# Performance work log

Hardware: AMD Instinct MI355X
Metric: run time of the kernel (lower is better)

Reference implementation:

```python
import jax, jax.numpy as jnp
import numpy as np

EPS_LN = 1e-5
EPS_STD = 1e-5


def _ln_dim1(z, g, b):
    # LayerNorm over channel dim (axis=1) of (B, C, T) or (B, C, 1)
    mu = z.mean(axis=1, keepdims=True)
    var = ((z - mu) ** 2).mean(axis=1, keepdims=True)
    return (z - mu) * jax.lax.rsqrt(var + EPS_LN) * g[None, :, None] + b[None, :, None]


def _stats(x, m):
    # weighted mean/std over time axis; m broadcasts over channels
    mean = (m * x).sum(axis=2)                                   # (B, C)
    std = jnp.sqrt(jnp.maximum((m * x * x).sum(axis=2) - mean ** 2, EPS_STD))
    return mean, std


def setup_inputs() -> dict:
    key = jax.random.key(0)
    ks = jax.random.split(key, 4)
    B, C, T, H = 16, 1536, 2000, 128
    x = jax.random.normal(ks[0], (B, C, T), dtype=jnp.float32)
    mask = jnp.ones((B, 1, T), dtype=jnp.float32)
    # attention MLP params (conv1x1 -> relu -> LN(dim=1) -> tanh -> conv1x1)
    w1 = jax.random.normal(ks[1], (H, 3 * C), dtype=jnp.float32) * (1.0 / np.sqrt(3 * C))
    b1 = jnp.zeros((H,), jnp.float32)
    g1 = jnp.ones((H,), jnp.float32)
    be1 = jnp.zeros((H,), jnp.float32)
    w2 = jax.random.normal(ks[2], (C, H), dtype=jnp.float32) * (1.0 / np.sqrt(H))
    b2 = jnp.zeros((C,), jnp.float32)
    g2 = jnp.ones((2 * C,), jnp.float32)
    be2 = jnp.zeros((2 * C,), jnp.float32)
    return {"x": x, "mask": mask, "w1": w1, "b1": b1, "g1": g1, "be1": be1,
            "w2": w2, "b2": b2, "g2": g2, "be2": be2}


def reference(x, mask, w1, b1, g1, be1, w2, b2, g2, be2):
    B, C, T = x.shape
    # time_attention: append masked global mean/std, broadcast over T
    total = mask.sum(axis=2, keepdims=True)                      # (B,1,1)
    mean0, std0 = _stats(x, mask / total)                        # (B,C)
    x_in = jnp.concatenate([
        x,
        jnp.broadcast_to(mean0[:, :, None], (B, C, T)),
        jnp.broadcast_to(std0[:, :, None], (B, C, T)),
    ], axis=1)                                                   # (B,3C,T)
    # attention MLP (conv1x1 == channel matmul)
    h = jnp.einsum("hc,bct->bht", w1, x_in) + b1[None, :, None]  # (B,H,T)
    h = jnp.tanh(_ln_dim1(jax.nn.relu(h), g1, be1))
    alpha = jnp.einsum("ch,bht->bct", w2, h) + b2[None, :, None]  # (B,C,T)
    # masked softmax over time
    alpha = jnp.where(mask == 0, -jnp.inf, alpha)
    alpha = jax.nn.softmax(alpha, axis=2)
    # attention-weighted stats
    mean, std = _stats(x, alpha)                                 # (B,C) each
    out = jnp.concatenate([mean, std], axis=1)[:, :, None]       # (B,2C,1)
    return _ln_dim1(out, g2, be2)
```

## Files before the change

kernel.cpp:

```cpp
#include <hip/hip_runtime.h>
#include <hip/hip_bf16.h>
#include <math.h>

constexpr int B_  = 16;
constexpr int C_  = 1536;
constexpr int T_  = 2000;
constexpr int H_  = 128;
constexpr int C3_ = 3 * C_;
constexpr int C2_ = 2 * C_;
constexpr int NT_ = 4;
constexpr int NTL_ = 32;

typedef short bf8 __attribute__((ext_vector_type(8)));
typedef short bf4 __attribute__((ext_vector_type(4)));
typedef float f4  __attribute__((ext_vector_type(4)));

__device__ inline unsigned short f2b(float f) {
  __bf16 h = (__bf16)f;
  return __builtin_bit_cast(unsigned short, h);
}

__global__ __launch_bounds__(256) void k_gemm1_stats(
    const float* __restrict__ x, const float* __restrict__ w1,
    const float* __restrict__ mask,
    float* __restrict__ h_pre, float* __restrict__ sp1, float* __restrict__ sp2) {
  __shared__ __align__(16) short As[2][128 * 32];
  __shared__ __align__(16) short Bs[2][64 * 32];
  const int b = blockIdx.y;
  const int tile = blockIdx.x;
  const int t0 = tile * 64;
  const int tid = threadIdx.x;
  const int lane = tid & 63;
  const int w = tid >> 6;
  const int l15 = lane & 15;
  const int l4 = lane >> 4;

  float4 va[4], vb[2];

  const int t4 = tid & 15;
  float mreg[4];
#pragma unroll
  for (int j = 0; j < 4; ++j) {
    int t = t0 + t4 * 4 + j;
    mreg[j] = (t < T_) ? mask[(size_t)b * T_ + t] : 0.f;
  }
  float* sp1row = sp1 + ((size_t)b * NTL_ + tile) * C_;
  float* sp2row = sp2 + ((size_t)b * NTL_ + tile) * C_;

  f4 acc[8];
#pragma unroll
  for (int mi = 0; mi < 8; ++mi) { f4 z = {0.f, 0.f, 0.f, 0.f}; acc[mi] = z; }

#define G1_GLOAD(K0)                                                          \
  {                                                                           \
    _Pragma("unroll")                                                         \
    for (int q = 0; q < 4; ++q) {                                             \
      int idx = q * 256 + tid;                                                \
      int row = idx >> 3, j4 = idx & 7;                                       \
      va[q] = *(const float4*)(w1 + (size_t)row * C3_ + (K0) + j4 * 4);       \
    }                                                                         \
    _Pragma("unroll")                                                         \
    for (int q = 0; q < 2; ++q) {                                             \
      int idx = q * 256 + tid;                                                \
      int k = idx >> 4;                                                       \
      int t = t0 + t4 * 4;                                                    \
      if (t < T_)                                                             \
        vb[q] = *(const float4*)(x + ((size_t)(b * C_ + (K0) + k)) * T_ + t); \
      else                                                                    \
        vb[q] = make_float4(0.f, 0.f, 0.f, 0.f);                              \
    }                                                                         \
  }
#define G1_LSTORE(BUF)                                                        \
  {                                                                           \
    _Pragma("unroll")                                                         \
    for (int q = 0; q < 4; ++q) {                                             \
      int idx = q * 256 + tid;                                                \
      int row = idx >> 3, j4 = idx & 7;                                       \
      int slot = (j4 >> 1) ^ ((row >> 2) & 3);                                \
      bf4 p;                                                                  \
      p[0] = (short)f2b(va[q].x); p[1] = (short)f2b(va[q].y);                 \
      p[2] = (short)f2b(va[q].z); p[3] = (short)f2b(va[q].w);                 \
      *(bf4*)&As[BUF][row * 32 + slot * 8 + (j4 & 1) * 4] = p;                \
    }                                                                         \
    _Pragma("unroll")                                                         \
    for (int q = 0; q < 2; ++q) {                                             \
      int idx = q * 256 + tid;                                                \
      int k = idx >> 4;                                                       \
      float vv[4] = {vb[q].x, vb[q].y, vb[q].z, vb[q].w};                     \
      _Pragma("unroll")                                                       \
      for (int j = 0; j < 4; ++j) {                                           \
        int row = t4 * 4 + j;                                                 \
        int slot = (k >> 3) ^ ((row >> 2) & 3);                               \
        Bs[BUF][row * 32 + slot * 8 + (k & 7)] = (short)f2b(vv[j]);           \
      }                                                                       \
    }                                                                         \
  }
#define G1_STATS(K0)                                                          \
  {                                                                           \
    _Pragma("unroll")                                                         \
    for (int q = 0; q < 2; ++q) {                                             \
      float vv[4] = {vb[q].x, vb[q].y, vb[q].z, vb[q].w};                     \
      float a1 = 0.f, a2 = 0.f;                                               \
      _Pragma("unroll")                                                       \
      for (int j = 0; j < 4; ++j) {                                           \
        float mx = mreg[j] * vv[j];                                           \
        a1 += mx;                                                             \
        a2 = fmaf(mx, vv[j], a2);                                             \
      }                                                                       \
      _Pragma("unroll")                                                       \
      for (int off = 1; off < 16; off <<= 1) {                                \
        a1 += __shfl_xor(a1, off);                                            \
        a2 += __shfl_xor(a2, off);                                            \
      }                                                                       \
      if (t4 == 0) {                                                          \
        int c = (K0) + q * 16 + (tid >> 4);                                   \
        sp1row[c] = a1;                                                       \
        sp2row[c] = a2;                                                       \
      }                                                                       \
    }                                                                         \
  }

  G1_GLOAD(0);
  G1_LSTORE(0);
  G1_STATS(0);
  __syncthreads();

  const int fA = (l15 >> 2) & 3;
  const int NS = C_ / 32;
  for (int s = 0; s < NS; ++s) {
    const int cur = s & 1;
    if (s + 1 < NS) G1_GLOAD((s + 1) * 32);
    {
      const int browB = w * 16 + l15;
      bf8 bfr = *(const bf8*)&Bs[cur][browB * 32 + (l4 ^ fA) * 8];
#pragma unroll
      for (int mi = 0; mi < 8; ++mi) {
        bf8 afr = *(const bf8*)&As[cur][(mi * 16 + l15) * 32 + (l4 ^ fA) * 8];
        acc[mi] = __builtin_amdgcn_mfma_f32_16x16x32_bf16(afr, bfr, acc[mi], 0, 0, 0);
      }
    }
    if (s + 1 < NS) {
      G1_LSTORE(cur ^ 1);
      G1_STATS((s + 1) * 32);
    }
    __syncthreads();
  }

  const int t = t0 + w * 16 + l15;
  if (t < T_) {
    float* dst = h_pre + ((size_t)b * T_ + t) * H_;
#pragma unroll
    for (int mi = 0; mi < 8; ++mi)
      *(f4*)&dst[mi * 16 + l4 * 4] = acc[mi];
  }
}

__global__ __launch_bounds__(256) void k_stats_reduce(
    const float* __restrict__ sp1, const float* __restrict__ sp2,
    const float* __restrict__ mask,
    float* __restrict__ mean0, float* __restrict__ std0) {
  __shared__ float rs[4];
  const int b = blockIdx.x / (C_ / 256);
  const int chunk = blockIdx.x % (C_ / 256);
  const int tid = threadIdx.x;
  const int lane = tid & 63;
  const int wv = tid >> 6;
  float sm = 0.f;
  for (int i = tid; i < T_; i += 256) sm += mask[(size_t)b * T_ + i];
#pragma unroll
  for (int off = 32; off; off >>= 1) sm += __shfl_xor(sm, off);
  if (lane == 0) rs[wv] = sm;
  __syncthreads();
  sm = rs[0] + rs[1] + rs[2] + rs[3];

  const int c = chunk * 256 + tid;
  float s1 = 0.f, s2 = 0.f;
#pragma unroll 8
  for (int tile = 0; tile < NTL_; ++tile) {
    const size_t j = ((size_t)b * NTL_ + tile) * C_ + c;
    s1 += sp1[j];
    s2 += sp2[j];
  }
  float mean = s1 / sm;
  float var = s2 / sm - mean * mean;
  mean0[b * C_ + c] = mean;
  std0[b * C_ + c] = sqrtf(fmaxf(var, 1e-5f));
}

__global__ __launch_bounds__(256) void k_hconst_wl1(
    const float* __restrict__ w1, const float* __restrict__ b1,
    const float* __restrict__ mean0, const float* __restrict__ std0,
    const float* __restrict__ w2,
    float* __restrict__ hconst, float* __restrict__ wl1) {
  const int wave = threadIdx.x >> 6;
  const int lane = threadIdx.x & 63;
  if (blockIdx.x < B_ * H_ / 4) {
    const int idx = blockIdx.x * 4 + wave;
    const int b = idx >> 7;
    const int h = idx & (H_ - 1);
    const float* wm  = w1 + (size_t)h * C3_ + C_;
    const float* wsd = wm + C_;
    const float* mn = mean0 + b * C_;
    const float* sd = std0 + b * C_;
    float s = 0.f;
    for (int c = lane; c < C_; c += 64)
      s += wm[c] * mn[c] + wsd[c] * sd[c];
#pragma unroll
    for (int off = 32; off; off >>= 1) s += __shfl_xor(s, off);
    if (lane == 0) hconst[idx] = s + b1[h];
  } else {
    const int c = (blockIdx.x - B_ * H_ / 4) * 4 + wave;
    const float* wr = w2 + (size_t)c * H_;
    float s = fabsf(wr[lane]) + fabsf(wr[lane + 64]);
#pragma unroll
    for (int off = 32; off; off >>= 1) s += __shfl_xor(s, off);
    if (lane == 0) wl1[c] = s;
  }
}

__global__ __launch_bounds__(256) void k_ln_epi(
    const float* __restrict__ h_pre, const float* __restrict__ hconst,
    const float* __restrict__ g1, const float* __restrict__ be1,
    unsigned short* __restrict__ hlnT) {
  const int b = blockIdx.y;
  const int t = blockIdx.x * 64 + (threadIdx.x >> 2);
  const int part = threadIdx.x & 3;
  if (t >= T_) return;
  const float* src = h_pre + ((size_t)b * T_ + t) * H_ + part * 32;
  const float* hc = hconst + b * H_ + part * 32;
  float v[32];
  float sum = 0.f, ssq = 0.f;
#pragma unroll
  for (int j = 0; j < 8; ++j) {
    float4 h4 = *(const float4*)(src + j * 4);
    float4 c4 = *(const float4*)(hc + j * 4);
    const float* hp = (const float*)&h4;
    const float* cp = (const float*)&c4;
#pragma unroll
    for (int r = 0; r < 4; ++r) {
      float u = fmaxf(hp[r] + cp[r], 0.f);
      v[j * 4 + r] = u;
      sum += u;
      ssq += u * u;
    }
  }
  sum += __shfl_xor(sum, 1); sum += __shfl_xor(sum, 2);
  ssq += __shfl_xor(ssq, 1); ssq += __shfl_xor(ssq, 2);
  const float mean = sum * (1.f / 128.f);
  const float rstd = rsqrtf(ssq * (1.f / 128.f) - mean * mean + 1e-5f);
  unsigned short* dst = hlnT + ((size_t)b * T_ + t) * H_ + part * 32;
  const float* gp = g1 + part * 32;
  const float* ep = be1 + part * 32;
#pragma unroll
  for (int m = 0; m < 4; ++m) {
    bf8 p;
#pragma unroll
    for (int r = 0; r < 8; ++r) {
      int j = m * 8 + r;
      p[r] = (short)f2b(tanhf((v[j] - mean) * rstd * gp[j] + ep[j]));
    }
    *(bf8*)&dst[m * 8] = p;
  }
}

__global__ __launch_bounds__(256) void k_gemm2_pool(
    const float* __restrict__ x, const float* __restrict__ mask,
    const float* __restrict__ w2, const unsigned short* __restrict__ hlnT,
    const float* __restrict__ wl1,
    float* __restrict__ ps0, float* __restrict__ ps1, float* __restrict__ ps2) {
  __shared__ __align__(16) short Hs[2][64 * 128];
  const int b = blockIdx.y;
  const int c0 = blockIdx.x * 128;
  const int part = blockIdx.z;
  const int tb = part * 512;
  const int te = min(tb + 512, T_);
  const int tid = threadIdx.x;
  const int lane = tid & 63;
  const int w = tid >> 6;
  const int l15 = lane & 15;
  const int l4 = lane >> 4;

  bf8 af[2][4];
#pragma unroll
  for (int mi = 0; mi < 2; ++mi)
#pragma unroll
    for (int ks = 0; ks < 4; ++ks) {
      const float* src = w2 + (size_t)(c0 + w * 32 + mi * 16 + l15) * H_ + (ks * 4 + l4) * 8;
      float4 v0 = *(const float4*)src;
      float4 v1 = *(const float4*)(src + 4);
      bf8 p;
      p[0] = (short)f2b(v0.x); p[1] = (short)f2b(v0.y);
      p[2] = (short)f2b(v0.z); p[3] = (short)f2b(v0.w);
      p[4] = (short)f2b(v1.x); p[5] = (short)f2b(v1.y);
      p[6] = (short)f2b(v1.z); p[7] = (short)f2b(v1.w);
      af[mi][ks] = p;
    }

  float Mc[8];
#pragma unroll
  for (int mi = 0; mi < 2; ++mi) {
    float4 m4 = *(const float4*)(wl1 + c0 + w * 32 + mi * 16 + l4 * 4);
    Mc[mi * 4 + 0] = m4.x; Mc[mi * 4 + 1] = m4.y;
    Mc[mi * 4 + 2] = m4.z; Mc[mi * 4 + 3] = m4.w;
  }

  float s0[8], s1[8], s2[8];
#pragma unroll
  for (int r = 0; r < 8; ++r) { s0[r] = 0.f; s1[r] = 0.f; s2[r] = 0.f; }

  bf8 hreg[4];
#define G2_HLOAD(T0)                                                          \
  {                                                                           \
    _Pragma("unroll")                                                         \
    for (int q = 0; q < 4; ++q) {                                             \
      int idx = q * 256 + tid;                                                \
      int row = idx >> 4, slot = idx & 15;                                    \
      int t = (T0) + row;                                                     \
      if (t > T_ - 1) t = T_ - 1;                                             \
      hreg[q] = *(const bf8*)(hlnT + ((size_t)b * T_ + t) * H_ + slot * 8);   \
    }                                                                         \
  }
#define G2_HSTORE(BUF)                                                        \
  {                                                                           \
    _Pragma("unroll")                                                         \
    for (int q = 0; q < 4; ++q) {                                             \
      int idx = q * 256 + tid;                                                \
      int row = idx >> 4, slot = idx & 15;                                    \
      *(bf8*)&Hs[BUF][row * 128 + (slot ^ (row & 15)) * 8] = hreg[q];         \
    }                                                                         \
  }

  G2_HLOAD(tb);
  G2_HSTORE(0);
  __syncthreads();

  const int NCH = (te - tb + 63) / 64;
  for (int ch = 0; ch < NCH; ++ch) {
    const int t0 = tb + ch * 64;
    const int cur = ch & 1;
    if (ch + 1 < NCH) G2_HLOAD(t0 + 64);

    float mk[4];
    int tcol[4];
#pragma unroll
    for (int nj = 0; nj < 4; ++nj) {
      int t = t0 + nj * 16 + l15;
      tcol[nj] = (t < T_) ? t : (T_ - 1);
      mk[nj] = (t < T_) ? mask[(size_t)b * T_ + t] : 0.f;
    }
    float xv[8][4];
#pragma unroll
    for (int mi = 0; mi < 2; ++mi)
#pragma unroll
      for (int reg = 0; reg < 4; ++reg) {
        const int c = c0 + w * 32 + mi * 16 + l4 * 4 + reg;
        const float* xrow = x + ((size_t)(b * C_ + c)) * T_;
#pragma unroll
        for (int nj = 0; nj < 4; ++nj) xv[mi * 4 + reg][nj] = xrow[tcol[nj]];
      }

    f4 acc[2][4];
#pragma unroll
    for (int mi = 0; mi < 2; ++mi)
#pragma unroll
      for (int nj = 0; nj < 4; ++nj) { f4 z = {0.f, 0.f, 0.f, 0.f}; acc[mi][nj] = z; }

#pragma unroll
    for (int ks = 0; ks < 4; ++ks) {
      const int sw = (ks * 4 + l4) ^ l15;
      bf8 bb[4];
#pragma unroll
      for (int nj = 0; nj < 4; ++nj)
        bb[nj] = *(const bf8*)&Hs[cur][(nj * 16 + l15) * 128 + sw * 8];
#pragma unroll
      for (int nj = 0; nj < 4; ++nj) {
        acc[0][nj] = __builtin_amdgcn_mfma_f32_16x16x32_bf16(af[0][ks], bb[nj], acc[0][nj], 0, 0, 0);
        acc[1][nj] = __builtin_amdgcn_mfma_f32_16x16x32_bf16(af[1][ks], bb[nj], acc[1][nj], 0, 0, 0);
      }
    }

#pragma unroll
    for (int mi = 0; mi < 2; ++mi)
#pragma unroll
      for (int reg = 0; reg < 4; ++reg) {
        const int r = mi * 4 + reg;
        float a0 = s0[r], a1 = s1[r], a2 = s2[r];
#pragma unroll
        for (int nj = 0; nj < 4; ++nj) {
          float e = (mk[nj] != 0.f) ? __expf(acc[mi][nj][reg] - Mc[r]) : 0.f;
          float xvv = xv[r][nj];
          a0 += e; a1 += e * xvv; a2 += e * xvv * xvv;
        }
        s0[r] = a0; s1[r] = a1; s2[r] = a2;
      }

    if (ch + 1 < NCH) G2_HSTORE(cur ^ 1);
    __syncthreads();
  }

#pragma unroll
  for (int off = 1; off < 16; off <<= 1) {
#pragma unroll
    for (int r = 0; r < 8; ++r) {
      s0[r] += __shfl_xor(s0[r], off);
      s1[r] += __shfl_xor(s1[r], off);
      s2[r] += __shfl_xor(s2[r], off);
    }
  }
  if (l15 == 0) {
#pragma unroll
    for (int mi = 0; mi < 2; ++mi)
#pragma unroll
      for (int reg = 0; reg < 4; ++reg) {
        const int r = mi * 4 + reg;
        const int c = c0 + w * 32 + mi * 16 + l4 * 4 + reg;
        const size_t j = ((size_t)(b * NT_ + part)) * C_ + c;
        ps0[j] = s0[r]; ps1[j] = s1[r]; ps2[j] = s2[r];
      }
  }
}

__global__ __launch_bounds__(256) void k_pool_merge(
    const float* __restrict__ ps0, const float* __restrict__ ps1,
    const float* __restrict__ ps2, float* __restrict__ pooled) {
  const int idx = blockIdx.x * 256 + threadIdx.x;
  const int b = idx / C_;
  const int c = idx - b * C_;
  float s0 = 0.f, s1 = 0.f, s2 = 0.f;
#pragma unroll
  for (int p = 0; p < NT_; ++p) {
    const size_t j = ((size_t)(b * NT_ + p)) * C_ + c;
    s0 += ps0[j]; s1 += ps1[j]; s2 += ps2[j];
  }
  float mean = s1 / s0;
  float var = s2 / s0 - mean * mean;
  pooled[b * C2_ + c] = mean;
  pooled[b * C2_ + C_ + c] = sqrtf(fmaxf(var, 1e-5f));
}

__global__ __launch_bounds__(256) void k_final_ln(
    const float* __restrict__ pooled, const float* __restrict__ g2,
    const float* __restrict__ be2, float* __restrict__ out) {
  __shared__ float rs[8];
  const int b = blockIdx.x;
  const int tid = threadIdx.x;
  const int lane = tid & 63;
  const int wave = tid >> 6;
  const float* p = pooled + b * C2_;
  float s = 0.f, q = 0.f;
  for (int i = tid; i < C2_; i += 256) {
    float v = p[i];
    s += v;
    q += v * v;
  }
#pragma unroll
  for (int off = 32; off; off >>= 1) {
    s += __shfl_xor(s, off);
    q += __shfl_xor(q, off);
  }
  if (lane == 0) { rs[wave] = s; rs[4 + wave] = q; }
  __syncthreads();
  s = rs[0] + rs[1] + rs[2] + rs[3];
  q = rs[4] + rs[5] + rs[6] + rs[7];
  float mean = s * (1.f / C2_);
  float var = q * (1.f / C2_) - mean * mean;
  float rstd = rsqrtf(var + 1e-5f);
  for (int i = tid; i < C2_; i += 256)
    out[b * C2_ + i] = (p[i] - mean) * rstd * g2[i] + be2[i];
}

extern "C" void kernel_launch(void* const* d_in, const int* in_sizes, int n_in,
                              void* d_out, int out_size, void* d_ws, size_t ws_size,
                              hipStream_t stream) {
  const float* x    = (const float*)d_in[0];
  const float* mask = (const float*)d_in[1];
  const float* w1   = (const float*)d_in[2];
  const float* b1   = (const float*)d_in[3];
  const float* g1   = (const float*)d_in[4];
  const float* be1  = (const float*)d_in[5];
  const float* w2   = (const float*)d_in[6];
  const float* g2   = (const float*)d_in[8];
  const float* be2  = (const float*)d_in[9];
  float* out = (float*)d_out;

  float* ws     = (float*)d_ws;
  float* mean0  = ws;
  float* std0   = mean0 + B_ * C_;
  float* hconst = std0 + B_ * C_;
  float* pooled = hconst + B_ * H_;
  float* wl1    = pooled + B_ * C2_;
  float* ps0    = wl1 + C_;
  float* ps1    = ps0 + B_ * NT_ * C_;
  float* ps2    = ps1 + B_ * NT_ * C_;
  float* sp1    = ps2 + B_ * NT_ * C_;
  float* sp2    = sp1 + B_ * NTL_ * C_;
  float* h_pre  = sp2 + B_ * NTL_ * C_;
  unsigned short* hlnT = (unsigned short*)(h_pre + (size_t)B_ * T_ * H_);

  k_gemm1_stats<<<dim3(NTL_, B_), dim3(256), 0, stream>>>(x, w1, mask, h_pre, sp1, sp2);
  k_stats_reduce<<<dim3(B_ * C_ / 256), dim3(256), 0, stream>>>(sp1, sp2, mask, mean0, std0);
  k_hconst_wl1<<<dim3(B_ * H_ / 4 + C_ / 4), dim3(256), 0, stream>>>(
      w1, b1, mean0, std0, w2, hconst, wl1);
  k_ln_epi<<<dim3(NTL_, B_), dim3(256), 0, stream>>>(h_pre, hconst, g1, be1, hlnT);
  k_gemm2_pool<<<dim3(C_ / 128, B_, NT_), dim3(256), 0, stream>>>(x, mask, w2, hlnT, wl1,
                                                                  ps0, ps1, ps2);
  k_pool_merge<<<dim3(B_ * C_ / 256), dim3(256), 0, stream>>>(ps0, ps1, ps2, pooled);
  k_final_ln<<<dim3(B_), dim3(256), 0, stream>>>(pooled, g2, be2, out);
}
```

Measured before the change: 164.9 us.

## Split GEMM1 over K halves and halve GEMM2 channel tile for more blocks

GEMM1 gets a second grid dimension that splits the channel reduction in two, with each half writing its own partial h_pre buffer. The LayerNorm epilogue sums the two partials. GEMM2 processes 64 channels per block instead of 128, doubling the grid. Both changes aim to raise occupancy and CU utilisation, since the old grids (512 and 768 blocks) underfill the GPU. The cost is extra h_pre traffic, an extra read in the epilogue, and reloading the H tile for twice as many blocks in GEMM2.

```diff
diff --git a/kernel.cpp b/kernel.cpp
--- a/kernel.cpp
+++ b/kernel.cpp
@@ -10,6 +10,7 @@
 constexpr int C2_ = 2 * C_;
 constexpr int NT_ = 4;
 constexpr int NTL_ = 32;
+constexpr int KH_ = C_ / 2;
 
 typedef short bf8 __attribute__((ext_vector_type(8)));
 typedef short bf4 __attribute__((ext_vector_type(4)));
@@ -28,6 +29,7 @@
   __shared__ __align__(16) short Bs[2][64 * 32];
   const int b = blockIdx.y;
   const int tile = blockIdx.x;
+  const int kbase = blockIdx.z * KH_;
   const int t0 = tile * 64;
   const int tid = threadIdx.x;
   const int lane = tid & 63;
@@ -120,16 +122,16 @@
     }                                                                         \
   }
 
-  G1_GLOAD(0);
+  G1_GLOAD(kbase);
   G1_LSTORE(0);
-  G1_STATS(0);
+  G1_STATS(kbase);
   __syncthreads();
 
   const int fA = (l15 >> 2) & 3;
-  const int NS = C_ / 32;
+  const int NS = KH_ / 32;
   for (int s = 0; s < NS; ++s) {
     const int cur = s & 1;
-    if (s + 1 < NS) G1_GLOAD((s + 1) * 32);
+    if (s + 1 < NS) G1_GLOAD(kbase + (s + 1) * 32);
     {
       const int browB = w * 16 + l15;
       bf8 bfr = *(const bf8*)&Bs[cur][browB * 32 + (l4 ^ fA) * 8];
@@ -141,14 +143,14 @@
     }
     if (s + 1 < NS) {
       G1_LSTORE(cur ^ 1);
-      G1_STATS((s + 1) * 32);
+      G1_STATS(kbase + (s + 1) * 32);
     }
     __syncthreads();
   }
 
   const int t = t0 + w * 16 + l15;
   if (t < T_) {
-    float* dst = h_pre + ((size_t)b * T_ + t) * H_;
+    float* dst = h_pre + (size_t)blockIdx.z * B_ * T_ * H_ + ((size_t)b * T_ + t) * H_;
 #pragma unroll
     for (int mi = 0; mi < 8; ++mi)
       *(f4*)&dst[mi * 16 + l4 * 4] = acc[mi];
@@ -226,19 +228,22 @@
   const int t = blockIdx.x * 64 + (threadIdx.x >> 2);
   const int part = threadIdx.x & 3;
   if (t >= T_) return;
-  const float* src = h_pre + ((size_t)b * T_ + t) * H_ + part * 32;
+  const float* srcA = h_pre + ((size_t)b * T_ + t) * H_ + part * 32;
+  const float* srcB = srcA + (size_t)B_ * T_ * H_;
   const float* hc = hconst + b * H_ + part * 32;
   float v[32];
   float sum = 0.f, ssq = 0.f;
 #pragma unroll
   for (int j = 0; j < 8; ++j) {
-    float4 h4 = *(const float4*)(src + j * 4);
+    float4 hA = *(const float4*)(srcA + j * 4);
+    float4 hB = *(const float4*)(srcB + j * 4);
     float4 c4 = *(const float4*)(hc + j * 4);
-    const float* hp = (const float*)&h4;
+    const float* pa = (const float*)&hA;
+    const float* pb = (const float*)&hB;
     const float* cp = (const float*)&c4;
 #pragma unroll
     for (int r = 0; r < 4; ++r) {
-      float u = fmaxf(hp[r] + cp[r], 0.f);
+      float u = fmaxf(pa[r] + pb[r] + cp[r], 0.f);
       v[j * 4 + r] = u;
       sum += u;
       ssq += u * u;
@@ -270,7 +275,7 @@
     float* __restrict__ ps0, float* __restrict__ ps1, float* __restrict__ ps2) {
   __shared__ __align__(16) short Hs[2][64 * 128];
   const int b = blockIdx.y;
-  const int c0 = blockIdx.x * 128;
+  const int c0 = blockIdx.x * 64;
   const int part = blockIdx.z;
   const int tb = part * 512;
   const int te = min(tb + 512, T_);
@@ -280,33 +285,29 @@
   const int l15 = lane & 15;
   const int l4 = lane >> 4;
 
-  bf8 af[2][4];
-#pragma unroll
-  for (int mi = 0; mi < 2; ++mi)
-#pragma unroll
-    for (int ks = 0; ks < 4; ++ks) {
-      const float* src = w2 + (size_t)(c0 + w * 32 + mi * 16 + l15) * H_ + (ks * 4 + l4) * 8;
-      float4 v0 = *(const float4*)src;
-      float4 v1 = *(const float4*)(src + 4);
-      bf8 p;
-      p[0] = (short)f2b(v0.x); p[1] = (short)f2b(v0.y);
-      p[2] = (short)f2b(v0.z); p[3] = (short)f2b(v0.w);
-      p[4] = (short)f2b(v1.x); p[5] = (short)f2b(v1.y);
-      p[6] = (short)f2b(v1.z); p[7] = (short)f2b(v1.w);
-      af[mi][ks] = p;
-    }
-
-  float Mc[8];
-#pragma unroll
-  for (int mi = 0; mi < 2; ++mi) {
-    float4 m4 = *(const float4*)(wl1 + c0 + w * 32 + mi * 16 + l4 * 4);
-    Mc[mi * 4 + 0] = m4.x; Mc[mi * 4 + 1] = m4.y;
-    Mc[mi * 4 + 2] = m4.z; Mc[mi * 4 + 3] = m4.w;
-  }
-
-  float s0[8], s1[8], s2[8];
-#pragma unroll
-  for (int r = 0; r < 8; ++r) { s0[r] = 0.f; s1[r] = 0.f; s2[r] = 0.f; }
+  bf8 af[4];
+#pragma unroll
+  for (int ks = 0; ks < 4; ++ks) {
+    const float* src = w2 + (size_t)(c0 + w * 16 + l15) * H_ + (ks * 4 + l4) * 8;
+    float4 v0 = *(const float4*)src;
+    float4 v1 = *(const float4*)(src + 4);
+    bf8 p;
+    p[0] = (short)f2b(v0.x); p[1] = (short)f2b(v0.y);
+    p[2] = (short)f2b(v0.z); p[3] = (short)f2b(v0.w);
+    p[4] = (short)f2b(v1.x); p[5] = (short)f2b(v1.y);
+    p[6] = (short)f2b(v1.z); p[7] = (short)f2b(v1.w);
+    af[ks] = p;
+  }
+
+  float Mc[4];
+  {
+    float4 m4 = *(const float4*)(wl1 + c0 + w * 16 + l4 * 4);
+    Mc[0] = m4.x; Mc[1] = m4.y; Mc[2] = m4.z; Mc[3] = m4.w;
+  }
+
+  float s0[4], s1[4], s2[4];
+#pragma unroll
+  for (int r = 0; r < 4; ++r) { s0[r] = 0.f; s1[r] = 0.f; s2[r] = 0.f; }
 
   bf8 hreg[4];
 #define G2_HLOAD(T0)                                                          \
@@ -348,22 +349,18 @@
       tcol[nj] = (t < T_) ? t : (T_ - 1);
       mk[nj] = (t < T_) ? mask[(size_t)b * T_ + t] : 0.f;
     }
-    float xv[8][4];
-#pragma unroll
-    for (int mi = 0; mi < 2; ++mi)
-#pragma unroll
-      for (int reg = 0; reg < 4; ++reg) {
-        const int c = c0 + w * 32 + mi * 16 + l4 * 4 + reg;
-        const float* xrow = x + ((size_t)(b * C_ + c)) * T_;
-#pragma unroll
-        for (int nj = 0; nj < 4; ++nj) xv[mi * 4 + reg][nj] = xrow[tcol[nj]];
-      }
-
-    f4 acc[2][4];
-#pragma unroll
-    for (int mi = 0; mi < 2; ++mi)
-#pragma unroll
-      for (int nj = 0; nj < 4; ++nj) { f4 z = {0.f, 0.f, 0.f, 0.f}; acc[mi][nj] = z; }
+    float xv[4][4];
+#pragma unroll
+    for (int reg = 0; reg < 4; ++reg) {
+      const int c = c0 + w * 16 + l4 * 4 + reg;
+      const float* xrow = x + ((size_t)(b * C_ + c)) * T_;
+#pragma unroll
+      for (int nj = 0; nj < 4; ++nj) xv[reg][nj] = xrow[tcol[nj]];
+    }
+
+    f4 acc[4];
+#pragma unroll
+    for (int nj = 0; nj < 4; ++nj) { f4 z = {0.f, 0.f, 0.f, 0.f}; acc[nj] = z; }
 
 #pragma unroll
     for (int ks = 0; ks < 4; ++ks) {
@@ -373,26 +370,21 @@
       for (int nj = 0; nj < 4; ++nj)
         bb[nj] = *(const bf8*)&Hs[cur][(nj * 16 + l15) * 128 + sw * 8];
 #pragma unroll
+      for (int nj = 0; nj < 4; ++nj)
+        acc[nj] = __builtin_amdgcn_mfma_f32_16x16x32_bf16(af[ks], bb[nj], acc[nj], 0, 0, 0);
+    }
+
+#pragma unroll
+    for (int reg = 0; reg < 4; ++reg) {
+      float a0 = s0[reg], a1 = s1[reg], a2 = s2[reg];
+#pragma unroll
       for (int nj = 0; nj < 4; ++nj) {
-        acc[0][nj] = __builtin_amdgcn_mfma_f32_16x16x32_bf16(af[0][ks], bb[nj], acc[0][nj], 0, 0, 0);
-        acc[1][nj] = __builtin_amdgcn_mfma_f32_16x16x32_bf16(af[1][ks], bb[nj], acc[1][nj], 0, 0, 0);
+        float e = (mk[nj] != 0.f) ? __expf(acc[nj][reg] - Mc[reg]) : 0.f;
+        float xvv = xv[reg][nj];
+        a0 += e; a1 += e * xvv; a2 += e * xvv * xvv;
       }
-    }
-
-#pragma unroll
-    for (int mi = 0; mi < 2; ++mi)
-#pragma unroll
-      for (int reg = 0; reg < 4; ++reg) {
-        const int r = mi * 4 + reg;
-        float a0 = s0[r], a1 = s1[r], a2 = s2[r];
-#pragma unroll
-        for (int nj = 0; nj < 4; ++nj) {
-          float e = (mk[nj] != 0.f) ? __expf(acc[mi][nj][reg] - Mc[r]) : 0.f;
-          float xvv = xv[r][nj];
-          a0 += e; a1 += e * xvv; a2 += e * xvv * xvv;
-        }
-        s0[r] = a0; s1[r] = a1; s2[r] = a2;
-      }
+      s0[reg] = a0; s1[reg] = a1; s2[reg] = a2;
+    }
 
     if (ch + 1 < NCH) G2_HSTORE(cur ^ 1);
     __syncthreads();
@@ -401,7 +393,7 @@
 #pragma unroll
   for (int off = 1; off < 16; off <<= 1) {
 #pragma unroll
-    for (int r = 0; r < 8; ++r) {
+    for (int r = 0; r < 4; ++r) {
       s0[r] += __shfl_xor(s0[r], off);
       s1[r] += __shfl_xor(s1[r], off);
       s2[r] += __shfl_xor(s2[r], off);
@@ -409,14 +401,11 @@
   }
   if (l15 == 0) {
 #pragma unroll
-    for (int mi = 0; mi < 2; ++mi)
-#pragma unroll
-      for (int reg = 0; reg < 4; ++reg) {
-        const int r = mi * 4 + reg;
-        const int c = c0 + w * 32 + mi * 16 + l4 * 4 + reg;
-        const size_t j = ((size_t)(b * NT_ + part)) * C_ + c;
-        ps0[j] = s0[r]; ps1[j] = s1[r]; ps2[j] = s2[r];
-      }
+    for (int reg = 0; reg < 4; ++reg) {
+      const int c = c0 + w * 16 + l4 * 4 + reg;
+      const size_t j = ((size_t)(b * NT_ + part)) * C_ + c;
+      ps0[j] = s0[reg]; ps1[j] = s1[reg]; ps2[j] = s2[reg];
+    }
   }
 }
 
@@ -495,15 +484,15 @@
   float* sp1    = ps2 + B_ * NT_ * C_;
   float* sp2    = sp1 + B_ * NTL_ * C_;
   float* h_pre  = sp2 + B_ * NTL_ * C_;
-  unsigned short* hlnT = (unsigned short*)(h_pre + (size_t)B_ * T_ * H_);
-
-  k_gemm1_stats<<<dim3(NTL_, B_), dim3(256), 0, stream>>>(x, w1, mask, h_pre, sp1, sp2);
+  unsigned short* hlnT = (unsigned short*)(h_pre + 2 * (size_t)B_ * T_ * H_);
+
+  k_gemm1_stats<<<dim3(NTL_, B_, 2), dim3(256), 0, stream>>>(x, w1, mask, h_pre, sp1, sp2);
   k_stats_reduce<<<dim3(B_ * C_ / 256), dim3(256), 0, stream>>>(sp1, sp2, mask, mean0, std0);
   k_hconst_wl1<<<dim3(B_ * H_ / 4 + C_ / 4), dim3(256), 0, stream>>>(
       w1, b1, mean0, std0, w2, hconst, wl1);
   k_ln_epi<<<dim3(NTL_, B_), dim3(256), 0, stream>>>(h_pre, hconst, g1, be1, hlnT);
-  k_gemm2_pool<<<dim3(C_ / 128, B_, NT_), dim3(256), 0, stream>>>(x, mask, w2, hlnT, wl1,
-                                                                  ps0, ps1, ps2);
+  k_gemm2_pool<<<dim3(C_ / 64, B_, NT_), dim3(256), 0, stream>>>(x, mask, w2, hlnT, wl1,
+                                                                 ps0, ps1, ps2);
   k_pool_merge<<<dim3(B_ * C_ / 256), dim3(256), 0, stream>>>(ps0, ps1, ps2, pooled);
   k_final_ln<<<dim3(B_), dim3(256), 0, stream>>>(pooled, g2, be2, out);
 }
```

Result: faster. 161.2 us (-2.2%).
